# Optimization experiments

Measured on AMD Instinct MI355X. Metric: run time of the kernel, lower is better.

Reference implementation:

```python
import jax, jax.numpy as jnp
import numpy as np

B, L, R, D, K, H = 512, 10, 2048, 256, 20, 128
VOCAB, GEO_V, GEO_D = 30000, 1000, 64

def _l2norm(x):
    # F.normalize(p=2, dim=-1): x / max(||x||, eps)
    return x / jnp.maximum(jnp.linalg.norm(x, axis=-1, keepdims=True), 1e-12)

def setup_inputs() -> dict:
    key = jax.random.key(0)
    ks = jax.random.split(key, 20)
    emb = 0.02 * jax.random.normal(ks[0], (VOCAB, D), jnp.float32)
    emb = emb.at[0].set(0.0)  # padding_idx=0 row is zero
    inp = {
        'text_left': jax.random.randint(ks[1], (B, L), 0, VOCAB),
        'text_right': jax.random.randint(ks[2], (B, R), 0, VOCAB),
        'location_left': jax.random.randint(ks[3], (B, 2), 0, GEO_V),
        'distance': jax.random.uniform(ks[4], (B,), jnp.float32),
        'emb': emb,
        'attn_w': 0.05 * jax.random.normal(ks[5], (D,), jnp.float32),
        'w_m0': 0.1 * jax.random.normal(ks[6], (K, H), jnp.float32),
        'b_m0': jnp.zeros((H,), jnp.float32),
        'w_m1': 0.1 * jax.random.normal(ks[7], (H, H), jnp.float32),
        'b_m1': jnp.zeros((H,), jnp.float32),
        'w_m2': 0.1 * jax.random.normal(ks[8], (H, 1), jnp.float32),
        'b_m2': jnp.zeros((1,), jnp.float32),
        'out_w': 0.5 * jax.random.normal(ks[9], (1, 1), jnp.float32),
        'out_b': jnp.zeros((1,), jnp.float32),
        'lat_tab': 0.05 * jax.random.normal(ks[10], (GEO_V, GEO_D), jnp.float32),
        'lon_tab': 0.05 * jax.random.normal(ks[11], (GEO_V, GEO_D), jnp.float32),
        'w3': 0.05 * jax.random.normal(ks[12], (D, 10), jnp.float32),
        'b3': jnp.zeros((10,), jnp.float32),
        'w5': 0.05 * jax.random.normal(ks[13], (GEO_D, 32), jnp.float32),
        'b5': jnp.zeros((32,), jnp.float32),
        'w4': 0.05 * jax.random.normal(ks[14], (164, 2), jnp.float32),
        'b4': jnp.zeros((2,), jnp.float32),
    }
    return inp

def reference(text_left, text_right, location_left, distance, emb, attn_w,
              w_m0, b_m0, w_m1, b_m1, w_m2, b_m2, out_w, out_b,
              lat_tab, lon_tab, w3, b3, w5, b5, w4, b4):
    # ---- no_grad block in the original ----
    mask_query = text_left == 0  # mask_value = 0
    embed_query = emb[text_left]            # [B,L,D]
    embed_doc = emb[text_right]             # [B,R,D]
    matching = jnp.einsum('bld,brd->blr', _l2norm(embed_query), _l2norm(embed_doc))
    topk = jax.lax.top_k(matching, K)[0]    # [B,L,K], sorted descending
    logits = jnp.einsum('bld,d->bl', embed_query, attn_w)
    logits = jnp.where(mask_query, -jnp.inf, logits)
    attn = jax.nn.softmax(logits, axis=-1)  # [B,L]
    h = jnp.tanh(topk @ w_m0 + b_m0)
    h = jnp.tanh(h @ w_m1 + b_m1)
    h = jnp.tanh(h @ w_m2 + b_m2)[..., 0]   # [B,L]
    x = jnp.einsum('bl,bl->b', h, attn)[:, None]  # [B,1]
    x = jnp.tanh(x @ out_w + out_b)         # out layer (tanh)
    x = jax.lax.stop_gradient(x)
    embed_query = jax.lax.stop_gradient(embed_query)
    # ---- trainable geo/weighting branch ----
    lat = lat_tab[location_left[:, 0]] @ w5 + b5   # [B,32]
    lon = lon_tab[location_left[:, 1]] @ w5 + b5   # [B,32]
    q1 = (embed_query @ w3 + b3).reshape(embed_query.shape[0], -1)  # [B,100]
    w = jnp.concatenate([q1, lat, lon], axis=-1) @ w4 + b4          # [B,2]
    x_all = jnp.concatenate([x, distance[:, None]], axis=1)         # [B,2]
    pred = jnp.sum(w * x_all, axis=1, keepdims=True)                # [B,1]
    return pred
```

## Files before the change

kernel.cpp:

```cpp
#include <hip/hip_runtime.h>
#include <hip/hip_fp16.h>
#include <math.h>

#define BB 512
#define LL 10
#define RR 2048
#define DD 256
#define KK 20
#define HH 128
#define NVOCAB 30000
#define GEOD 64

#define FP8_SCALE   64.0f
#define FP8_DESCALE (1.0f / 4096.0f)

#define EMB8_BYTES (NVOCAB * DD)
#define BLOB1_OFF  EMB8_BYTES
#define BLOB2_OFF  (BLOB1_OFF + 8192)
#define W3T_OFF    (BLOB2_OFF + 32768)
#define W5T_OFF    (W3T_OFF + 10240)

typedef __attribute__((ext_vector_type(2))) long long llx2;
typedef __attribute__((ext_vector_type(4))) float f32x4;
typedef __attribute__((ext_vector_type(8))) short bf16x8;

static __device__ inline unsigned short f2bf(float f) {
    unsigned u = __float_as_uint(f);
    unsigned r = (u + 0x7fff + ((u >> 16) & 1)) >> 16;
    return (unsigned short)r;
}

__global__ __launch_bounds__(256) void pre_kernel(
    const float* __restrict__ emb,
    const float* __restrict__ w_m0, const float* __restrict__ w_m1,
    const float* __restrict__ w3,   const float* __restrict__ w5,
    unsigned char* __restrict__ emb8,
    unsigned short* __restrict__ blob1, unsigned short* __restrict__ blob2,
    float* __restrict__ w3T, float* __restrict__ w5T)
{
    if (blockIdx.x < 7500) {
        int row  = blockIdx.x * 4 + (threadIdx.x >> 6);
        int lane = threadIdx.x & 63;
        int e0 = ((lane >> 1) & 7) * 32 + (lane >> 4) * 8 + (lane & 1) * 4;
        float4 v = *(const float4*)(emb + (size_t)row * DD + e0);
        float ssq = v.x * v.x + v.y * v.y + v.z * v.z + v.w * v.w;
        #pragma unroll
        for (int off = 32; off; off >>= 1) ssq += __shfl_xor(ssq, off);
        float s = FP8_SCALE / fmaxf(sqrtf(ssq), 1e-12f);
        unsigned pk = 0;
        pk = (unsigned)__builtin_amdgcn_cvt_pk_fp8_f32(v.x * s, v.y * s, (int)pk, false);
        pk = (unsigned)__builtin_amdgcn_cvt_pk_fp8_f32(v.z * s, v.w * s, (int)pk, true);
        ((unsigned*)(emb8 + (size_t)row * DD))[lane] = pk;
    } else {
        int i = (blockIdx.x - 7500) * 256 + threadIdx.x;
        if (i < 4096) {
            int t = i >> 9, ln = (i >> 3) & 63, tt = i & 7;
            int n = t * 16 + (ln & 15), k = (ln >> 4) * 8 + tt;
            blob1[i] = (k < KK) ? f2bf(w_m0[k * HH + n]) : (unsigned short)0;
        } else if (i < 4096 + 16384) {
            int i2 = i - 4096;
            int ks = i2 >> 12, rem = i2 & 4095;
            int t = rem >> 9, ln = (rem >> 3) & 63, tt = rem & 7;
            int n = t * 16 + (ln & 15), k = ks * 32 + (ln >> 4) * 8 + tt;
            blob2[i2] = f2bf(w_m1[k * HH + n]);
        } else if (i < 4096 + 16384 + 2560) {
            int i3 = i - (4096 + 16384);
            int j = i3 >> 8, d = i3 & 255;
            w3T[i3] = w3[d * 10 + j];
        } else if (i < 4096 + 16384 + 2560 + 2048) {
            int i4 = i - (4096 + 16384 + 2560);
            int c = i4 >> 6, d = i4 & 63;
            w5T[i4] = w5[d * 32 + c];
        }
    }
}

static __device__ inline unsigned wave_umax_u32(unsigned x)
{
    unsigned t;
    t = (unsigned)__builtin_amdgcn_update_dpp((int)x, (int)x, 0x111, 0xF, 0xF, false); x = x > t ? x : t;
    t = (unsigned)__builtin_amdgcn_update_dpp((int)x, (int)x, 0x112, 0xF, 0xF, false); x = x > t ? x : t;
    t = (unsigned)__builtin_amdgcn_update_dpp((int)x, (int)x, 0x114, 0xF, 0xF, false); x = x > t ? x : t;
    t = (unsigned)__builtin_amdgcn_update_dpp((int)x, (int)x, 0x118, 0xF, 0xF, false); x = x > t ? x : t;
    t = (unsigned)__builtin_amdgcn_update_dpp((int)x, (int)x, 0x142, 0xF, 0xF, false); x = x > t ? x : t;
    t = (unsigned)__builtin_amdgcn_update_dpp((int)x, (int)x, 0x143, 0xF, 0xF, false); x = x > t ? x : t;
    return (unsigned)__builtin_amdgcn_readlane((int)x, 63);
}

static __device__ inline void build_top2(const unsigned short* __restrict__ row,
                                         int lane, unsigned extmask,
                                         unsigned& k1, unsigned& k2)
{
    unsigned m1 = 0u, m2 = 0u;
    #pragma unroll
    for (int k = 0; k < 32; ++k) {
        int j = lane + 64 * k;
        unsigned key = ((unsigned)row[j] << 16) | (unsigned)(2047 - j);
        key = ((extmask >> k) & 1u) ? 0u : key;
        unsigned mn = m1 < key ? m1 : key;
        m1 = m1 > key ? m1 : key;
        m2 = m2 > mn ? m2 : mn;
    }
    k1 = m1; k2 = m2;
}

__global__ __launch_bounds__(512, 4) void fused_kernel(
    const int*   __restrict__ text_left,
    const int*   __restrict__ text_right,
    const int*   __restrict__ loc_left,
    const float* __restrict__ distance,
    const float* __restrict__ emb,
    const float* __restrict__ attn_w,
    const float* __restrict__ b_m0, const float* __restrict__ b_m1,
    const float* __restrict__ w_m2, const float* __restrict__ b_m2,
    const float* __restrict__ out_w, const float* __restrict__ out_b,
    const float* __restrict__ lat_tab, const float* __restrict__ lon_tab,
    const float* __restrict__ b3, const float* __restrict__ b5,
    const float* __restrict__ w4, const float* __restrict__ b4,
    const unsigned char*  __restrict__ emb8,
    const unsigned short* __restrict__ blob1,
    const unsigned short* __restrict__ blob2,
    const float* __restrict__ w3T, const float* __restrict__ w5T,
    float*       __restrict__ out)
{
    __shared__ __align__(16) unsigned char arena[32768];
    __shared__ __align__(16) unsigned short s_keys[LL][RR];
    __shared__ __align__(8) unsigned short s_docs[RR];
    __shared__ float s_logit[LL];
    __shared__ float s_h[16];
    __shared__ float s_feat[164];

    unsigned short* s_h1   = (unsigned short*)arena;
    float*          s_topk = (float*)(arena + 4096);

    const int b    = blockIdx.x;
    const int tid  = threadIdx.x;
    const int lane = tid & 63;
    const int wid  = tid >> 6;
    const int m15  = lane & 15, q = lane >> 4;

    {
        unsigned* s_cnt = (unsigned*)arena;
        unsigned* s_off = (unsigned*)(arena + 1024);
        if (tid < 256) s_cnt[tid] = 0u;
        __syncthreads();
        const int* trb = text_right + b * RR;
        int dv[4];
        #pragma unroll
        for (int i = 0; i < 4; ++i) {
            dv[i] = trb[tid * 4 + i];
            atomicAdd(&s_cnt[dv[i] >> 7], 1u);
        }
        __syncthreads();
        if (tid < 256) s_off[tid + 1] = s_cnt[tid];
        if (tid == 0) s_off[0] = 0u;
        __syncthreads();
        #pragma unroll 1
        for (int st = 1; st < 256; st <<= 1) {
            unsigned v = 0u;
            if (tid < 256 && tid + 1 > st) v = s_off[tid + 1 - st];
            __syncthreads();
            if (tid < 256 && tid + 1 > st) s_off[tid + 1] += v;
            __syncthreads();
        }
        #pragma unroll
        for (int i = 0; i < 4; ++i) {
            unsigned p = atomicAdd(&s_off[dv[i] >> 7], 1u);
            s_docs[p] = (unsigned short)dv[i];
        }
        __syncthreads();
    }

    {
        llx2 afr[4];
        {
            int qidx = (m15 < LL) ? text_left[b * LL + m15] : 0;
            const unsigned char* ap = emb8 + (size_t)qidx * DD + q * 64;
            #pragma unroll
            for (int s = 0; s < 4; ++s) afr[s] = *(const llx2*)(ap + s * 16);
        }
        const int r0 = lane >> 4;
        const int c  = lane & 15;

        unsigned char* stg = arena + wid * 4096;

        int  I[4];
        llx2 R[4];

        auto LOADI = [&](int i) {
            const unsigned short* p = s_docs + (wid + 8 * i) * 16 + r0;
            I[0] = p[0]; I[1] = p[4]; I[2] = p[8]; I[3] = p[12];
        };
        auto LOADR = [&]() {
            #pragma unroll
            for (int j = 0; j < 4; ++j)
                R[j] = *(const llx2*)(emb8 + (size_t)I[j] * DD + (c << 4));
        };
        auto STORE = [&]() {
            #pragma unroll
            for (int j = 0; j < 4; ++j) {
                int r = j * 4 + r0;
                *(llx2*)(stg + r * 256 + ((c ^ r) << 4)) = R[j];
            }
        };
        auto COMPUTE = [&](int i) {
            llx2 bf[4];
            #pragma unroll
            for (int s = 0; s < 4; ++s)
                bf[s] = *(const llx2*)(stg + m15 * 256 + (((q * 4 + s) ^ m15) << 4));
            f32x4 acc = {0.f, 0.f, 0.f, 0.f};
            #pragma unroll
            for (int s = 0; s < 4; ++s) {
                acc = __builtin_amdgcn_mfma_f32_16x16x32_fp8_fp8(afr[s][0], bf[s][0], acc, 0, 0, 0);
                acc = __builtin_amdgcn_mfma_f32_16x16x32_fp8_fp8(afr[s][1], bf[s][1], acc, 0, 0, 0);
            }
            int n0 = (wid + 8 * i) * 16;
            #pragma unroll
            for (int v = 0; v < 4; ++v) {
                int m = q * 4 + v;
                if (m < LL) {
                    float sc = acc[v] * FP8_DESCALE;
                    unsigned hb = (unsigned)__half_as_ushort(__float2half(sc));
                    unsigned ok = hb ^ ((hb & 0x8000u) ? 0xFFFFu : 0x8000u);
                    s_keys[m][n0 + m15] = (unsigned short)ok;
                }
            }
        };

        LOADI(0); LOADR(); LOADI(1);
        #pragma unroll 1
        for (int t = 0; t < 16; ++t) {
            STORE();
            if (t < 15) {
                LOADR();
                if (t < 14) LOADI(t + 2);
            }
            COMPUTE(t);
        }
    }
    __syncthreads();

    {
        int row = tid >> 5, col = tid & 31;
        if (row >= LL || col >= KK) s_topk[row * 32 + col] = 0.f;
    }

    {
        auto TOPK_ROW = [&](int l) {
            const unsigned short* krow = &s_keys[l][0];
            unsigned extmask = 0u, k1, k2;
            build_top2(krow, lane, extmask, k1, k2);
            #pragma unroll 1
            for (int it = 0; it < KK; ++it) {
                unsigned bmk = wave_umax_u32(k1);
                if (k1 == bmk) {
                    unsigned o16 = bmk >> 16;
                    unsigned hbv = (o16 & 0x8000u) ? (o16 & 0x7FFFu) : (o16 ^ 0xFFFFu);
                    s_topk[l * 32 + it] = __half2float(__ushort_as_half((unsigned short)hbv));
                    int j = 2047 - (int)(bmk & 0xFFFFu);
                    extmask |= 1u << (j >> 6);
                    k1 = k2; k2 = 0u;
                }
                if (__any(k1 == 0u)) {
                    if (k1 == 0u) build_top2(krow, lane, extmask, k1, k2);
                }
            }
        };
        TOPK_ROW(wid);
        if (wid >= 6) {
            TOPK_ROW(wid + 2);
        } else if (wid == 4) {
            const float4 aw = *(const float4*)(attn_w + lane * 4);
            for (int l = 0; l < LL; ++l) {
                int v = text_left[b * LL + l];
                float4 qv = *(const float4*)(emb + (size_t)v * DD + lane * 4);
                float d = qv.x * aw.x + qv.y * aw.y + qv.z * aw.z + qv.w * aw.w;
                #pragma unroll
                for (int off = 32; off; off >>= 1) d += __shfl_xor(d, off);
                if (lane == 0) s_logit[l] = (v == 0) ? -INFINITY : d;
            }
        } else if (wid == 5) {
            int c = lane & 31, which = lane >> 5;
            int v = loc_left[b * 2 + which];
            const float* tab = which ? lon_tab : lat_tab;
            const float4* tr = (const float4*)(tab + (size_t)v * GEOD);
            const float4* wr = (const float4*)(w5T + c * GEOD);
            float a = b5[c];
            #pragma unroll
            for (int d4 = 0; d4 < 16; ++d4) {
                float4 tv = tr[d4], wv = wr[d4];
                a += tv.x * wv.x + tv.y * wv.y + tv.z * wv.z + tv.w * wv.w;
            }
            s_feat[100 + which * 32 + c] = a;
        } else if (wid == 2 || wid == 3) {
            int p = (wid - 2) * 64 + lane;
            if (p < 100) {
                int l = p / 10, j = p % 10;
                int v = text_left[b * LL + l];
                const float4* qr = (const float4*)(emb + (size_t)v * DD);
                const float4* wr = (const float4*)(w3T + j * DD);
                float a = b3[j];
                #pragma unroll 8
                for (int d4 = 0; d4 < 64; ++d4) {
                    float4 qv = qr[d4], wv = wr[d4];
                    a += qv.x * wv.x + qv.y * wv.y + qv.z * wv.z + qv.w * wv.w;
                }
                s_feat[p] = a;
            }
        }
    }
    __syncthreads();

    if (wid == 0) {
        float tv[8];
        *(float4*)(tv)     = *(const float4*)(&s_topk[m15 * 32 + q * 8]);
        *(float4*)(tv + 4) = *(const float4*)(&s_topk[m15 * 32 + q * 8 + 4]);
        bf16x8 a1;
        #pragma unroll
        for (int t = 0; t < 8; ++t) a1[t] = (short)f2bf(tv[t]);
        f32x4 acc1[8];
        #pragma unroll
        for (int t = 0; t < 8; ++t) {
            bf16x8 b1 = *(const bf16x8*)(blob1 + t * 512 + lane * 8);
            f32x4 z = {0.f, 0.f, 0.f, 0.f};
            acc1[t] = __builtin_amdgcn_mfma_f32_16x16x32_bf16(a1, b1, z, 0, 0, 0);
        }
        #pragma unroll
        for (int t = 0; t < 8; ++t) {
            int c = t * 16 + m15;
            float bb0 = b_m0[c];
            #pragma unroll
            for (int v = 0; v < 4; ++v) {
                int m = q * 4 + v;
                float h = tanhf(acc1[t][v] + bb0);
                s_h1[m * 128 + (((c >> 3) ^ m) << 3) + (c & 7)] = f2bf(h);
            }
        }
        f32x4 acc2[8];
        #pragma unroll
        for (int t = 0; t < 8; ++t) acc2[t] = (f32x4){0.f, 0.f, 0.f, 0.f};
        #pragma unroll
        for (int ks = 0; ks < 4; ++ks) {
            bf16x8 a2 = *(const bf16x8*)(s_h1 + m15 * 128 + (((ks * 4 + q) ^ m15) << 3));
            #pragma unroll
            for (int t = 0; t < 8; ++t) {
                bf16x8 b2 = *(const bf16x8*)(blob2 + (ks * 8 + t) * 512 + lane * 8);
                acc2[t] = __builtin_amdgcn_mfma_f32_16x16x32_bf16(a2, b2, acc2[t], 0, 0, 0);
            }
        }
        float part[4] = {0.f, 0.f, 0.f, 0.f};
        #pragma unroll
        for (int t = 0; t < 8; ++t) {
            int c = t * 16 + m15;
            float bb1 = b_m1[c];
            float wm2 = w_m2[c];
            #pragma unroll
            for (int v = 0; v < 4; ++v)
                part[v] += tanhf(acc2[t][v] + bb1) * wm2;
        }
        #pragma unroll
        for (int v = 0; v < 4; ++v) {
            #pragma unroll
            for (int off = 1; off < 16; off <<= 1) part[v] += __shfl_xor(part[v], off);
        }
        if (m15 == 0) {
            #pragma unroll
            for (int v = 0; v < 4; ++v) {
                int m = q * 4 + v;
                if (m < LL) s_h[m] = tanhf(part[v] + b_m2[0]);
            }
        }
        float w0p = 0.f, w1p = 0.f;
        #pragma unroll
        for (int i = lane; i < 164; i += 64) {
            float f = s_feat[i];
            w0p += f * w4[i * 2 + 0];
            w1p += f * w4[i * 2 + 1];
        }
        #pragma unroll
        for (int off = 32; off; off >>= 1) {
            w0p += __shfl_xor(w0p, off);
            w1p += __shfl_xor(w1p, off);
        }
        if (lane == 0) {
            float mx = -INFINITY;
            #pragma unroll
            for (int l = 0; l < LL; ++l) mx = fmaxf(mx, s_logit[l]);
            float ex[LL];
            float sum = 0.f;
            #pragma unroll
            for (int l = 0; l < LL; ++l) { ex[l] = expf(s_logit[l] - mx); sum += ex[l]; }
            float x = 0.f;
            #pragma unroll
            for (int l = 0; l < LL; ++l) x += s_h[l] * (ex[l] / sum);
            float xo = tanhf(x * out_w[0] + out_b[0]);
            out[b] = (w0p + b4[0]) * xo + (w1p + b4[1]) * distance[b];
        }
    }
}

extern "C" void kernel_launch(void* const* d_in, const int* in_sizes, int n_in,
                              void* d_out, int out_size, void* d_ws, size_t ws_size,
                              hipStream_t stream) {
    const int*   text_left  = (const int*)  d_in[0];
    const int*   text_right = (const int*)  d_in[1];
    const int*   loc_left   = (const int*)  d_in[2];
    const float* distance   = (const float*)d_in[3];
    const float* emb        = (const float*)d_in[4];
    const float* attn_w     = (const float*)d_in[5];
    const float* w_m0       = (const float*)d_in[6];
    const float* b_m0       = (const float*)d_in[7];
    const float* w_m1       = (const float*)d_in[8];
    const float* b_m1       = (const float*)d_in[9];
    const float* w_m2       = (const float*)d_in[10];
    const float* b_m2       = (const float*)d_in[11];
    const float* out_w      = (const float*)d_in[12];
    const float* out_b      = (const float*)d_in[13];
    const float* lat_tab    = (const float*)d_in[14];
    const float* lon_tab    = (const float*)d_in[15];
    const float* w3         = (const float*)d_in[16];
    const float* b3         = (const float*)d_in[17];
    const float* w5         = (const float*)d_in[18];
    const float* b5         = (const float*)d_in[19];
    const float* w4         = (const float*)d_in[20];
    const float* b4         = (const float*)d_in[21];

    unsigned char*  ws    = (unsigned char*)d_ws;
    unsigned char*  emb8  = ws;
    unsigned short* blob1 = (unsigned short*)(ws + BLOB1_OFF);
    unsigned short* blob2 = (unsigned short*)(ws + BLOB2_OFF);
    float*          w3T   = (float*)(ws + W3T_OFF);
    float*          w5T   = (float*)(ws + W5T_OFF);
    float*          out   = (float*)d_out;

    pre_kernel<<<7598, 256, 0, stream>>>(emb, w_m0, w_m1, w3, w5,
                                         emb8, blob1, blob2, w3T, w5T);

    fused_kernel<<<BB, 512, 0, stream>>>(
        text_left, text_right, loc_left, distance, emb, attn_w,
        b_m0, b_m1, w_m2, b_m2, out_w, out_b,
        lat_tab, lon_tab, b3, b5, w4, b4,
        emb8, blob1, blob2, w3T, w5T, out);
}
```

Before: 55.46 us.

## Quantize normalized embeddings to FP4 and use scaled 16x16x128 MFMA

Replaces the FP8 normalized embedding table with a packed FP4 (e2m1) table and computes the query-doc similarity with the MX-scaled f8f6f4 MFMA at K=128. This halves the bytes gathered per doc row and the LDS staging footprint, and cuts the MFMA instruction count per tile. FP4 is much coarser than FP8, so the top-k selection over similarities may change, which risks accuracy beyond tolerance. The pre-kernel quantization also switches to a plain lane-contiguous layout with a branchy comparison-based encoder.

After: 51.02 us (median of 2 runs). -8.0%, faster.

```diff
diff --git a/kernel.cpp b/kernel.cpp
--- a/kernel.cpp
+++ b/kernel.cpp
@@ -11,11 +11,11 @@
 #define NVOCAB 30000
 #define GEOD 64
 
-#define FP8_SCALE   64.0f
-#define FP8_DESCALE (1.0f / 4096.0f)
-
-#define EMB8_BYTES (NVOCAB * DD)
-#define BLOB1_OFF  EMB8_BYTES
+#define FP4_SCALE   24.0f
+#define FP4_DESCALE (1.0f / 576.0f)
+
+#define EMB4_BYTES (NVOCAB * 128)
+#define BLOB1_OFF  EMB4_BYTES
 #define BLOB2_OFF  (BLOB1_OFF + 8192)
 #define W3T_OFF    (BLOB2_OFF + 32768)
 #define W5T_OFF    (W3T_OFF + 10240)
@@ -23,6 +23,7 @@
 typedef __attribute__((ext_vector_type(2))) long long llx2;
 typedef __attribute__((ext_vector_type(4))) float f32x4;
 typedef __attribute__((ext_vector_type(8))) short bf16x8;
+typedef __attribute__((ext_vector_type(8))) int   i32x8;
 
 static __device__ inline unsigned short f2bf(float f) {
     unsigned u = __float_as_uint(f);
@@ -30,27 +31,35 @@
     return (unsigned short)r;
 }
 
+static __device__ inline unsigned q_e2m1(float x) {
+    unsigned s = (x < 0.f) ? 8u : 0u;
+    float a = fabsf(x);
+    unsigned c = (a < 0.25f) ? 0u : (a < 0.75f) ? 1u : (a < 1.25f) ? 2u :
+                 (a < 1.75f) ? 3u : (a < 2.5f)  ? 4u : (a < 3.5f)  ? 5u :
+                 (a < 5.0f)  ? 6u : 7u;
+    return s | c;
+}
+
 __global__ __launch_bounds__(256) void pre_kernel(
     const float* __restrict__ emb,
     const float* __restrict__ w_m0, const float* __restrict__ w_m1,
     const float* __restrict__ w3,   const float* __restrict__ w5,
-    unsigned char* __restrict__ emb8,
+    unsigned char* __restrict__ emb4,
     unsigned short* __restrict__ blob1, unsigned short* __restrict__ blob2,
     float* __restrict__ w3T, float* __restrict__ w5T)
 {
     if (blockIdx.x < 7500) {
         int row  = blockIdx.x * 4 + (threadIdx.x >> 6);
         int lane = threadIdx.x & 63;
-        int e0 = ((lane >> 1) & 7) * 32 + (lane >> 4) * 8 + (lane & 1) * 4;
-        float4 v = *(const float4*)(emb + (size_t)row * DD + e0);
+        float4 v = *(const float4*)(emb + (size_t)row * DD + lane * 4);
         float ssq = v.x * v.x + v.y * v.y + v.z * v.z + v.w * v.w;
         #pragma unroll
         for (int off = 32; off; off >>= 1) ssq += __shfl_xor(ssq, off);
-        float s = FP8_SCALE / fmaxf(sqrtf(ssq), 1e-12f);
-        unsigned pk = 0;
-        pk = (unsigned)__builtin_amdgcn_cvt_pk_fp8_f32(v.x * s, v.y * s, (int)pk, false);
-        pk = (unsigned)__builtin_amdgcn_cvt_pk_fp8_f32(v.z * s, v.w * s, (int)pk, true);
-        ((unsigned*)(emb8 + (size_t)row * DD))[lane] = pk;
+        float s = FP4_SCALE / fmaxf(sqrtf(ssq), 1e-12f);
+        unsigned n0 = q_e2m1(v.x * s), n1 = q_e2m1(v.y * s);
+        unsigned n2 = q_e2m1(v.z * s), n3 = q_e2m1(v.w * s);
+        unsigned short pk = (unsigned short)(n0 | (n1 << 4) | (n2 << 8) | (n3 << 12));
+        ((unsigned short*)(emb4 + (size_t)row * 128))[lane] = pk;
     } else {
         int i = (blockIdx.x - 7500) * 256 + threadIdx.x;
         if (i < 4096) {
@@ -117,13 +126,13 @@
     const float* __restrict__ lat_tab, const float* __restrict__ lon_tab,
     const float* __restrict__ b3, const float* __restrict__ b5,
     const float* __restrict__ w4, const float* __restrict__ b4,
-    const unsigned char*  __restrict__ emb8,
+    const unsigned char*  __restrict__ emb4,
     const unsigned short* __restrict__ blob1,
     const unsigned short* __restrict__ blob2,
     const float* __restrict__ w3T, const float* __restrict__ w5T,
     float*       __restrict__ out)
 {
-    __shared__ __align__(16) unsigned char arena[32768];
+    __shared__ __align__(16) unsigned char arena[16384];
     __shared__ __align__(16) unsigned short s_keys[LL][RR];
     __shared__ __align__(8) unsigned short s_docs[RR];
     __shared__ float s_logit[LL];
@@ -172,54 +181,52 @@
     }
 
     {
-        llx2 afr[4];
+        i32x8 a0, a1;
         {
             int qidx = (m15 < LL) ? text_left[b * LL + m15] : 0;
-            const unsigned char* ap = emb8 + (size_t)qidx * DD + q * 64;
-            #pragma unroll
-            for (int s = 0; s < 4; ++s) afr[s] = *(const llx2*)(ap + s * 16);
-        }
-        const int r0 = lane >> 4;
-        const int c  = lane & 15;
-
-        unsigned char* stg = arena + wid * 4096;
-
-        int  I[4];
-        llx2 R[4];
+            const unsigned char* ap = emb4 + (size_t)qidx * 128;
+            uint4 f0 = *(const uint4*)(ap + q * 16);
+            uint4 f1 = *(const uint4*)(ap + 64 + q * 16);
+            a0 = (i32x8){(int)f0.x, (int)f0.y, (int)f0.z, (int)f0.w, 0, 0, 0, 0};
+            a1 = (i32x8){(int)f1.x, (int)f1.y, (int)f1.z, (int)f1.w, 0, 0, 0, 0};
+        }
+        const int r0 = lane >> 3;
+        const int c  = lane & 7;
+
+        unsigned char* stg = arena + wid * 2048;
+
+        int  I0, I1;
+        llx2 R0, R1;
 
         auto LOADI = [&](int i) {
-            const unsigned short* p = s_docs + (wid + 8 * i) * 16 + r0;
-            I[0] = p[0]; I[1] = p[4]; I[2] = p[8]; I[3] = p[12];
+            int T = wid + 8 * i;
+            I0 = (int)s_docs[T * 16 + r0];
+            I1 = (int)s_docs[T * 16 + 8 + r0];
         };
         auto LOADR = [&]() {
-            #pragma unroll
-            for (int j = 0; j < 4; ++j)
-                R[j] = *(const llx2*)(emb8 + (size_t)I[j] * DD + (c << 4));
+            R0 = *(const llx2*)(emb4 + (size_t)I0 * 128 + (c << 4));
+            R1 = *(const llx2*)(emb4 + (size_t)I1 * 128 + (c << 4));
         };
         auto STORE = [&]() {
-            #pragma unroll
-            for (int j = 0; j < 4; ++j) {
-                int r = j * 4 + r0;
-                *(llx2*)(stg + r * 256 + ((c ^ r) << 4)) = R[j];
-            }
+            *(llx2*)(stg + r0 * 128 + ((c ^ r0) << 4))       = R0;
+            *(llx2*)(stg + (8 + r0) * 128 + ((c ^ r0) << 4)) = R1;
         };
         auto COMPUTE = [&](int i) {
-            llx2 bf[4];
-            #pragma unroll
-            for (int s = 0; s < 4; ++s)
-                bf[s] = *(const llx2*)(stg + m15 * 256 + (((q * 4 + s) ^ m15) << 4));
+            uint4 b0 = *(const uint4*)(stg + m15 * 128 + ((q ^ (m15 & 7)) << 4));
+            uint4 b1 = *(const uint4*)(stg + m15 * 128 + (((4 + q) ^ (m15 & 7)) << 4));
+            i32x8 bb0 = {(int)b0.x, (int)b0.y, (int)b0.z, (int)b0.w, 0, 0, 0, 0};
+            i32x8 bb1 = {(int)b1.x, (int)b1.y, (int)b1.z, (int)b1.w, 0, 0, 0, 0};
             f32x4 acc = {0.f, 0.f, 0.f, 0.f};
-            #pragma unroll
-            for (int s = 0; s < 4; ++s) {
-                acc = __builtin_amdgcn_mfma_f32_16x16x32_fp8_fp8(afr[s][0], bf[s][0], acc, 0, 0, 0);
-                acc = __builtin_amdgcn_mfma_f32_16x16x32_fp8_fp8(afr[s][1], bf[s][1], acc, 0, 0, 0);
-            }
+            acc = __builtin_amdgcn_mfma_scale_f32_16x16x128_f8f6f4(
+                      a0, bb0, acc, 4, 4, 0, 0x7F7F7F7F, 0, 0x7F7F7F7F);
+            acc = __builtin_amdgcn_mfma_scale_f32_16x16x128_f8f6f4(
+                      a1, bb1, acc, 4, 4, 0, 0x7F7F7F7F, 0, 0x7F7F7F7F);
             int n0 = (wid + 8 * i) * 16;
             #pragma unroll
             for (int v = 0; v < 4; ++v) {
                 int m = q * 4 + v;
                 if (m < LL) {
-                    float sc = acc[v] * FP8_DESCALE;
+                    float sc = acc[v] * FP4_DESCALE;
                     unsigned hb = (unsigned)__half_as_ushort(__float2half(sc));
                     unsigned ok = hb ^ ((hb & 0x8000u) ? 0xFFFFu : 0x8000u);
                     s_keys[m][n0 + m15] = (unsigned short)ok;
@@ -280,18 +287,18 @@
                 if (lane == 0) s_logit[l] = (v == 0) ? -INFINITY : d;
             }
         } else if (wid == 5) {
-            int c = lane & 31, which = lane >> 5;
+            int c2 = lane & 31, which = lane >> 5;
             int v = loc_left[b * 2 + which];
             const float* tab = which ? lon_tab : lat_tab;
             const float4* tr = (const float4*)(tab + (size_t)v * GEOD);
-            const float4* wr = (const float4*)(w5T + c * GEOD);
-            float a = b5[c];
+            const float4* wr = (const float4*)(w5T + c2 * GEOD);
+            float a = b5[c2];
             #pragma unroll
             for (int d4 = 0; d4 < 16; ++d4) {
                 float4 tv = tr[d4], wv = wr[d4];
                 a += tv.x * wv.x + tv.y * wv.y + tv.z * wv.z + tv.w * wv.w;
             }
-            s_feat[100 + which * 32 + c] = a;
+            s_feat[100 + which * 32 + c2] = a;
         } else if (wid == 2 || wid == 3) {
             int p = (wid - 2) * 64 + lane;
             if (p < 100) {
@@ -426,7 +433,7 @@
     const float* b4         = (const float*)d_in[21];
 
     unsigned char*  ws    = (unsigned char*)d_ws;
-    unsigned char*  emb8  = ws;
+    unsigned char*  emb4  = ws;
     unsigned short* blob1 = (unsigned short*)(ws + BLOB1_OFF);
     unsigned short* blob2 = (unsigned short*)(ws + BLOB2_OFF);
     float*          w3T   = (float*)(ws + W3T_OFF);
@@ -434,11 +441,11 @@
     float*          out   = (float*)d_out;
 
     pre_kernel<<<7598, 256, 0, stream>>>(emb, w_m0, w_m1, w3, w5,
-                                         emb8, blob1, blob2, w3T, w5T);
+                                         emb4, blob1, blob2, w3T, w5T);
 
     fused_kernel<<<BB, 512, 0, stream>>>(
         text_left, text_right, loc_left, distance, emb, attn_w,
         b_m0, b_m1, w_m2, b_m2, out_w, out_b,
         lat_tab, lon_tab, b3, b5, w4, b4,
-        emb8, blob1, blob2, w3T, w5T, out);
-}
+        emb4, blob1, blob2, w3T, w5T, out);
+}
```
